# Performance work log

Measured on AMD Instinct MI355X. Metric: run time of the kernel, lower is better.

## Reference

```python
import jax, jax.numpy as jnp
import numpy as np

B, I, H = 8192, 1024, 1024

def setup_inputs() -> dict:
    key = jax.random.key(0)
    ks = jax.random.split(key, 5)
    # xavier-uniform-ish scale for weights
    sW = float(np.sqrt(6.0 / (I + H)))
    sU = float(np.sqrt(6.0 / (H + H)))
    return {
        "x": jax.random.normal(ks[0], (B, I), jnp.float32),
        "h": jax.random.normal(ks[1], (B, H), jnp.float32),
        "c": jax.random.normal(ks[2], (B, H), jnp.float32),
        # gate order along leading axis: 0=i, 1=f, 2=o, 3=c_hat
        "W": jax.random.uniform(ks[3], (4, H, I), jnp.float32, -sW, sW),
        "bW": jnp.zeros((4, H), jnp.float32),
        "U": jax.random.uniform(ks[4], (4, H, H), jnp.float32, -sU, sU),
        "bU": jnp.zeros((4, H), jnp.float32),
    }

def reference(x, h, c, W, bW, U, bU):
    # two batched GEMMs covering all 8 original Linear layers
    gx = jnp.einsum('bi,ghi->gbh', x, W) + bW[:, None, :]   # [4,B,H]
    gh = jnp.einsum('bk,ghk->gbh', h, U) + bU[:, None, :]   # [4,B,H]
    g = gx + gh
    i = jax.nn.sigmoid(g[0])
    f = jax.nn.sigmoid(g[1])
    o = jax.nn.sigmoid(g[2])
    c_hat = jnp.tanh(g[3])
    c_new = f * c + i * c_hat
    h_new = o * jnp.tanh(c_new)
    return (h_new, (h_new, c_new))
```

## Files before the change

kernel.cpp:

```cpp
#include <hip/hip_runtime.h>
#include <hip/hip_bf16.h>

typedef __hip_bfloat16 bf16;
typedef __attribute__((ext_vector_type(8))) short short8;
typedef __attribute__((ext_vector_type(4))) short short4v;
typedef __attribute__((ext_vector_type(4))) float floatx4;

#define B_DIM 8192
#define H_DIM 1024
#define KSUM 2048
#define BM 256
#define BN 256
#define BK 64
#define KT 32
#define NSLOT 10
#define SLOT_ELEMS 8192
#define CEX_STRIDE 68

union BS { bf16 b; short s; };
__device__ __forceinline__ short cvt1(float f) {
  BS u; u.b = __float2bfloat16(f); return u.s;
}
__device__ __forceinline__ short4v cvt4(float4 v) {
  short4v r;
  r[0] = cvt1(v.x); r[1] = cvt1(v.y); r[2] = cvt1(v.z); r[3] = cvt1(v.w);
  return r;
}

__device__ __forceinline__ void async_ld16(const bf16* g, bf16* lds) {
  __builtin_amdgcn_global_load_lds(
      (const __attribute__((address_space(1))) unsigned int*)g,
      (__attribute__((address_space(3))) unsigned int*)lds,
      16, 0, 0);
}

#define NX_UNITS 2097152
#define NW_UNITS 1048576
#define TOT_UNITS 6291456
__global__ __launch_bounds__(256) void cvt_pack(
    const float* __restrict__ x, const float* __restrict__ h,
    const float* __restrict__ W, const float* __restrict__ U,
    bf16* __restrict__ Ac, bf16* __restrict__ Bc) {
  const float4* const x4 = (const float4*)x;
  const float4* const h4 = (const float4*)h;
  const float4* const W4 = (const float4*)W;
  const float4* const U4 = (const float4*)U;
  short4v* const Ac4 = (short4v*)Ac;
  short4v* const Bc4 = (short4v*)Bc;

  const int stride = gridDim.x * 256;
  for (long u = blockIdx.x * 256 + threadIdx.x; u < TOT_UNITS; u += stride) {
    if (u < NX_UNITS) {
      const long r = u >> 8; const int c = (int)(u & 255);
      Ac4[r * 512 + c] = cvt4(x4[u]);
    } else if (u < 2 * NX_UNITS) {
      const long v = u - NX_UNITS;
      const long r = v >> 8; const int c = (int)(v & 255);
      Ac4[r * 512 + 256 + c] = cvt4(h4[v]);
    } else if (u < 2 * NX_UNITS + NW_UNITS) {
      const long w = u - 2 * NX_UNITS;
      const int g = (int)(w >> 18); const long hh = (w >> 8) & 1023;
      const int c = (int)(w & 255);
      Bc4[(hh * 4 + g) * 512 + c] = cvt4(W4[w]);
    } else {
      const long w = u - (2 * NX_UNITS + NW_UNITS);
      const int g = (int)(w >> 18); const long hh = (w >> 8) & 1023;
      const int c = (int)(w & 255);
      Bc4[(hh * 4 + g) * 512 + 256 + c] = cvt4(U4[w]);
    }
  }
}

__device__ __forceinline__ float sigmoidf_(float v) {
  return 1.0f / (1.0f + __expf(-v));
}
__device__ __forceinline__ float tanhf_(float v) {
  return 1.0f - 2.0f / (__expf(2.0f * v) + 1.0f);
}
__device__ __forceinline__ float getc(const float4& v, int t) {
  return t == 0 ? v.x : t == 1 ? v.y : t == 2 ? v.z : v.w;
}

__global__ __launch_bounds__(512, 2) void gemm_lstm(
    const bf16* __restrict__ Ac, const bf16* __restrict__ Bc,
    const float* __restrict__ cprev_g, const float* __restrict__ bW,
    const float* __restrict__ bU, float* __restrict__ out) {
  extern __shared__ __align__(16) char smem[];
  bf16* const ring = (bf16*)smem;
  float* const cex = (float*)smem;

  const int tid  = threadIdx.x;
  const int lane = tid & 63;
  const int wv   = tid >> 6;
  const int wm_idx = wv >> 2;
  const int wn_idx = wv & 3;

  const int blk  = blockIdx.x;
  const int xcd  = blk & 7;
  const int slot = blk >> 3;
  const int mt   = slot & 31;
  const int nt   = (xcd << 1) | (slot >> 5);
  const long m0 = (long)mt * BM;
  const long n0 = (long)nt * BN;

  const int lrow   = lane >> 3;
  const int lchunk = lane & 7;
  const int schunk = lchunk ^ lrow;
  const bf16* const aRow0 = Ac + (m0 + wv * 8 + lrow) * (long)KSUM + schunk * 8;
  const bf16* const bRow0 = Bc + (n0 + wv * 8 + lrow) * (long)KSUM + schunk * 8;

  const int col16 = lane & 15;
  const int quad  = lane >> 4;
  const int x7    = col16 & 7;
  const int bRowOff = (wn_idx & 1) << 6;

  floatx4 acc[8][4];
#pragma unroll
  for (int i = 0; i < 8; ++i)
#pragma unroll
    for (int jq = 0; jq < 4; ++jq) acc[i][jq] = (floatx4){0.f, 0.f, 0.f, 0.f};

#define STAGE_HALF(h_)                                                        \
  {                                                                           \
    const int c_ = (h_) & 3;                                                  \
    const long off_ = ((long)((c_ >> 1) * 128)) * KSUM + (long)(((h_) >> 2) * BK); \
    const bf16* s_ = ((c_ & 1) ? bRow0 : aRow0) + off_;                       \
    bf16* d_ = ring + ((h_) % NSLOT) * SLOT_ELEMS + wv * 512;                 \
    async_ld16(s_, d_);                                                       \
    async_ld16(s_ + 64L * KSUM, d_ + 4096);                                   \
  }

#define STAGE_P(p_)                                                           \
  { const int h_ = 4 * j + (p_) + 6; if (h_ < 4 * KT) STAGE_HALF(h_); }

#define RD_A(dst, rh_, s_)                                                    \
  _Pragma("unroll") for (int fi = 0; fi < 4; ++fi)                            \
    dst[fi] = *(const short8*)&rA[((rh_) * 64 + fi * 16 + col16) * 64 +       \
                                  (((((s_) << 2) + quad) ^ x7) << 3)];

#define RD_B(dst, s_)                                                         \
  _Pragma("unroll") for (int fj = 0; fj < 4; ++fj)                            \
    dst[fj] = *(const short8*)&rB[(bRowOff + fj * 16 + col16) * 64 +          \
                                  (((((s_) << 2) + quad) ^ x7) << 3)];

#define MM(accrow_, a_, b_)                                                   \
  __builtin_amdgcn_s_setprio(1);                                              \
  _Pragma("unroll") for (int fi = 0; fi < 4; ++fi)                            \
    _Pragma("unroll") for (int fj = 0; fj < 4; ++fj)                          \
      acc[(accrow_) + fi][fj] = __builtin_amdgcn_mfma_f32_16x16x32_bf16(      \
          a_[fi], b_[fj], acc[(accrow_) + fi][fj], 0, 0, 0);                  \
  __builtin_amdgcn_s_setprio(0);

#define FENCE() __builtin_amdgcn_sched_barrier(0)

#pragma unroll
  for (int h = 0; h < 6; ++h) STAGE_HALF(h);
  asm volatile("s_waitcnt vmcnt(4)" ::: "memory");
  __builtin_amdgcn_s_barrier();

#pragma unroll 1
  for (int j = 0; j < KT; ++j) {
    const bf16* const rA =
        ring + ((4 * j + 2 * wm_idx) % NSLOT) * SLOT_ELEMS;
    const bf16* const rB =
        ring + ((4 * j + 1 + ((wn_idx >> 1) << 1)) % NSLOT) * SLOT_ELEMS;
    short8 a0s0[4], a0s1[4], a1s0[4], a1s1[4], b_s0[4], b_s1[4];

    RD_A(a0s0, 0, 0) RD_B(b_s0, 0)
    FENCE();
    RD_A(a0s1, 0, 1) RD_B(b_s1, 1)
    FENCE();
    STAGE_P(0) STAGE_P(1)
    FENCE();
    MM(0, a0s0, b_s0)
    FENCE();
    RD_A(a1s0, 1, 0)
    FENCE();
    MM(0, a0s1, b_s1)
    FENCE();
    RD_A(a1s1, 1, 1)
    STAGE_P(2) STAGE_P(3)
    FENCE();
    MM(4, a1s0, b_s0)
    MM(4, a1s1, b_s1)
    if (j < KT - 2) asm volatile("s_waitcnt vmcnt(4)" ::: "memory");
    else            asm volatile("s_waitcnt vmcnt(0)" ::: "memory");
    __builtin_amdgcn_s_barrier();
  }

  const int rquad = (lane >> 4) << 2;
  const int row16 = lane & 15;
  const int tq    = lane >> 4;
  const long hglob = ((n0 + (long)(wn_idx << 6)) >> 2) + tq * 4;

  float4 bsum[4];
#pragma unroll
  for (int g = 0; g < 4; ++g) {
    const float4 a = *(const float4*)(bW + g * H_DIM + hglob);
    const float4 b = *(const float4*)(bU + g * H_DIM + hglob);
    bsum[g] = (float4){a.x + b.x, a.y + b.y, a.z + b.z, a.w + b.w};
  }

  float* wx = cex + wv * (16 * CEX_STRIDE);
  const long BH = (long)B_DIM * H_DIM;

#pragma unroll
  for (int ig = 0; ig < 8; ++ig) {
#pragma unroll
    for (int jj = 0; jj < 4; ++jj)
#pragma unroll
      for (int r = 0; r < 4; ++r)
        wx[(rquad + r) * CEX_STRIDE + jj * 16 + col16] = acc[ig][jj][r];

    float4 g4[4];
#pragma unroll
    for (int t = 0; t < 4; ++t)
      g4[t] = *(const float4*)&wx[row16 * CEX_STRIDE + (tq * 4 + t) * 4];

    const long mrow = m0 + (long)wm_idx * 128 + ig * 16 + row16;
    const float4 cp4 = *(const float4*)(cprev_g + mrow * H_DIM + hglob);

    float hn[4], cn[4];
#pragma unroll
    for (int t = 0; t < 4; ++t) {
      const float gi = g4[t].x + getc(bsum[0], t);
      const float gf = g4[t].y + getc(bsum[1], t);
      const float go = g4[t].z + getc(bsum[2], t);
      const float gg = g4[t].w + getc(bsum[3], t);
      const float I = sigmoidf_(gi);
      const float F = sigmoidf_(gf);
      const float O = sigmoidf_(go);
      const float G = tanhf_(gg);
      const float cv = F * getc(cp4, t) + I * G;
      hn[t] = O * tanhf_(cv);
      cn[t] = cv;
    }
    const float4 hn4 = {hn[0], hn[1], hn[2], hn[3]};
    const float4 cn4 = {cn[0], cn[1], cn[2], cn[3]};
    const long ob = mrow * H_DIM + hglob;
    *(float4*)(out + ob)          = hn4;
    *(float4*)(out + BH + ob)     = hn4;
    *(float4*)(out + 2 * BH + ob) = cn4;
  }
}

extern "C" void kernel_launch(void* const* d_in, const int* in_sizes, int n_in,
                              void* d_out, int out_size, void* d_ws, size_t ws_size,
                              hipStream_t stream) {
  const float* x  = (const float*)d_in[0];
  const float* h  = (const float*)d_in[1];
  const float* c  = (const float*)d_in[2];
  const float* W  = (const float*)d_in[3];
  const float* bW = (const float*)d_in[4];
  const float* U  = (const float*)d_in[5];
  const float* bU = (const float*)d_in[6];
  float* out = (float*)d_out;

  bf16* Ac = (bf16*)d_ws;
  bf16* Bc = (bf16*)((char*)d_ws + (size_t)33554432);

  static bool attr_done = false;
  if (!attr_done) {
    hipFuncSetAttribute(reinterpret_cast<const void*>(gemm_lstm),
                        hipFuncAttributeMaxDynamicSharedMemorySize, 163840);
    attr_done = true;
  }

  cvt_pack<<<4096, 256, 0, stream>>>(x, h, W, U, Ac, Bc);
  gemm_lstm<<<512, 512, 163840, stream>>>(Ac, Bc, c, bW, bU, out);
}
```

Baseline: 333.4 us.

## Shrink GEMM tile to 256x128 with BK=32 and 4-wave blocks

Changes the fused GEMM+LSTM kernel from 256x256 tiles with 8 waves and BK=64 to 256x128 tiles with 4 waves and BK=32. This doubles the grid to 1024 blocks and rebuilds the LDS ring: 9 slots of 3 buffers (A0, A1, B) with a new swizzled staging layout and fragment addressing. The goal is smaller LDS use (73.7KB) for more resident blocks and better CU balance. In exchange, B is reused across fewer rows, so global/L2 traffic per FLOP rises, and a barrier is hit every 32-wide K step. The epilogue is not shown and may not match the new wave layout.

```diff
diff --git a/kernel.cpp b/kernel.cpp
--- a/kernel.cpp
+++ b/kernel.cpp
@@ -10,11 +10,11 @@
 #define H_DIM 1024
 #define KSUM 2048
 #define BM 256
-#define BN 256
-#define BK 64
-#define KT 32
-#define NSLOT 10
-#define SLOT_ELEMS 8192
+#define BN 128
+#define BK 32
+#define KT 64
+#define NSLOT 9
+#define SLOT_ELEMS 4096
 #define CEX_STRIDE 68
 
 union BS { bf16 b; short s; };
@@ -81,7 +81,7 @@
   return t == 0 ? v.x : t == 1 ? v.y : t == 2 ? v.z : v.w;
 }
 
-__global__ __launch_bounds__(512, 2) void gemm_lstm(
+__global__ __launch_bounds__(256, 2) void gemm_lstm(
     const bf16* __restrict__ Ac, const bf16* __restrict__ Bc,
     const float* __restrict__ cprev_g, const float* __restrict__ bW,
     const float* __restrict__ bU, float* __restrict__ out) {
@@ -92,27 +92,27 @@
   const int tid  = threadIdx.x;
   const int lane = tid & 63;
   const int wv   = tid >> 6;
-  const int wm_idx = wv >> 2;
-  const int wn_idx = wv & 3;
+  const int wm_idx = wv >> 1;
+  const int wn_idx = wv & 1;
 
   const int blk  = blockIdx.x;
   const int xcd  = blk & 7;
   const int slot = blk >> 3;
   const int mt   = slot & 31;
-  const int nt   = (xcd << 1) | (slot >> 5);
+  const int nt   = (xcd << 2) | (slot >> 5);
   const long m0 = (long)mt * BM;
   const long n0 = (long)nt * BN;
 
-  const int lrow   = lane >> 3;
-  const int lchunk = lane & 7;
-  const int schunk = lchunk ^ lrow;
-  const bf16* const aRow0 = Ac + (m0 + wv * 8 + lrow) * (long)KSUM + schunk * 8;
-  const bf16* const bRow0 = Bc + (n0 + wv * 8 + lrow) * (long)KSUM + schunk * 8;
+  const int rbits = 2 * (lane >> 3) + ((lane >> 2) & 1);
+  const int csrc  = (lane & 3) ^ ((lane >> 3) & 3);
+  const bf16* const aStage = Ac + (m0 + wv * 32 + rbits) * (long)KSUM + csrc * 8;
+  const bf16* const bStage = Bc + (n0 + wv * 32 + rbits) * (long)KSUM + csrc * 8;
 
   const int col16 = lane & 15;
   const int quad  = lane >> 4;
-  const int x7    = col16 & 7;
-  const int bRowOff = (wn_idx & 1) << 6;
+  const int c16h  = col16 >> 1;
+  const int c16l  = col16 & 1;
+  const int loff  = c16h * 64 + c16l * 32 + ((quad ^ (c16h & 3)) << 3);
 
   floatx4 acc[8][4];
 #pragma unroll
@@ -120,72 +120,67 @@
 #pragma unroll
     for (int jq = 0; jq < 4; ++jq) acc[i][jq] = (floatx4){0.f, 0.f, 0.f, 0.f};
 
-#define STAGE_HALF(h_)                                                        \
+#define STAGE_SLOT(kt_, c_, sl_)                                              \
   {                                                                           \
-    const int c_ = (h_) & 3;                                                  \
-    const long off_ = ((long)((c_ >> 1) * 128)) * KSUM + (long)(((h_) >> 2) * BK); \
-    const bf16* s_ = ((c_ & 1) ? bRow0 : aRow0) + off_;                       \
-    bf16* d_ = ring + ((h_) % NSLOT) * SLOT_ELEMS + wv * 512;                 \
+    const bf16* s_ = (((c_) == 2) ? bStage                                    \
+                                  : (aStage + (long)(c_) * 128 * KSUM)) +     \
+                     (long)(kt_) * BK;                                        \
+    bf16* d_ = ring + (sl_) * SLOT_ELEMS + wv * 1024;                         \
     async_ld16(s_, d_);                                                       \
-    async_ld16(s_ + 64L * KSUM, d_ + 4096);                                   \
-  }
-
-#define STAGE_P(p_)                                                           \
-  { const int h_ = 4 * j + (p_) + 6; if (h_ < 4 * KT) STAGE_HALF(h_); }
-
-#define RD_A(dst, rh_, s_)                                                    \
+    async_ld16(s_ + 16L * KSUM, d_ + 512);                                    \
+  }
+
+#define RD_A4(lo_)                                                            \
   _Pragma("unroll") for (int fi = 0; fi < 4; ++fi)                            \
-    dst[fi] = *(const short8*)&rA[((rh_) * 64 + fi * 16 + col16) * 64 +       \
-                                  (((((s_) << 2) + quad) ^ x7) << 3)];
-
-#define RD_B(dst, s_)                                                         \
+    af[(lo_) + fi] = *(const short8*)&rA[((lo_) + fi) * 512 + loff];
+
+#define RD_B4()                                                               \
   _Pragma("unroll") for (int fj = 0; fj < 4; ++fj)                            \
-    dst[fj] = *(const short8*)&rB[(bRowOff + fj * 16 + col16) * 64 +          \
-                                  (((((s_) << 2) + quad) ^ x7) << 3)];
-
-#define MM(accrow_, a_, b_)                                                   \
+    bfr[fj] = *(const short8*)&rB[wn_idx * 2048 + fj * 512 + loff];
+
+#define MM16(lo_)                                                             \
   __builtin_amdgcn_s_setprio(1);                                              \
   _Pragma("unroll") for (int fi = 0; fi < 4; ++fi)                            \
     _Pragma("unroll") for (int fj = 0; fj < 4; ++fj)                          \
-      acc[(accrow_) + fi][fj] = __builtin_amdgcn_mfma_f32_16x16x32_bf16(      \
-          a_[fi], b_[fj], acc[(accrow_) + fi][fj], 0, 0, 0);                  \
+      acc[(lo_) + fi][fj] = __builtin_amdgcn_mfma_f32_16x16x32_bf16(          \
+          af[(lo_) + fi], bfr[fj], acc[(lo_) + fi][fj], 0, 0, 0);             \
   __builtin_amdgcn_s_setprio(0);
 
 #define FENCE() __builtin_amdgcn_sched_barrier(0)
 
 #pragma unroll
-  for (int h = 0; h < 6; ++h) STAGE_HALF(h);
-  asm volatile("s_waitcnt vmcnt(4)" ::: "memory");
+  for (int kt = 0; kt < 2; ++kt)
+#pragma unroll
+    for (int c = 0; c < 3; ++c)
+      STAGE_SLOT(kt, c, 3 * kt + c)
+  asm volatile("s_waitcnt vmcnt(6)" ::: "memory");
   __builtin_amdgcn_s_barrier();
 
+  int sb = 0;
 #pragma unroll 1
   for (int j = 0; j < KT; ++j) {
-    const bf16* const rA =
-        ring + ((4 * j + 2 * wm_idx) % NSLOT) * SLOT_ELEMS;
-    const bf16* const rB =
-        ring + ((4 * j + 1 + ((wn_idx >> 1) << 1)) % NSLOT) * SLOT_ELEMS;
-    short8 a0s0[4], a0s1[4], a1s0[4], a1s1[4], b_s0[4], b_s1[4];
-
-    RD_A(a0s0, 0, 0) RD_B(b_s0, 0)
+    const bf16* const rA = ring + (sb + wm_idx) * SLOT_ELEMS;
+    const bf16* const rB = ring + (sb + 2) * SLOT_ELEMS;
+    short8 af[8], bfr[4];
+
+    RD_B4() RD_A4(0) RD_A4(4)
     FENCE();
-    RD_A(a0s1, 0, 1) RD_B(b_s1, 1)
+    {
+      const int w = (sb >= 3) ? sb - 3 : sb + 6;
+      if (j + 2 < KT) {
+        STAGE_SLOT(j + 2, 0, w)
+        STAGE_SLOT(j + 2, 1, w + 1)
+        STAGE_SLOT(j + 2, 2, w + 2)
+      }
+    }
     FENCE();
-    STAGE_P(0) STAGE_P(1)
+    MM16(0)
     FENCE();
-    MM(0, a0s0, b_s0)
-    FENCE();
-    RD_A(a1s0, 1, 0)
-    FENCE();
-    MM(0, a0s1, b_s1)
-    FENCE();
-    RD_A(a1s1, 1, 1)
-    STAGE_P(2) STAGE_P(3)
-    FENCE();
-    MM(4, a1s0, b_s0)
-    MM(4, a1s1, b_s1)
-    if (j < KT - 2) asm volatile("s_waitcnt vmcnt(4)" ::: "memory");
+    MM16(4)
+    if (j < KT - 2) asm volatile("s_waitcnt vmcnt(6)" ::: "memory");
     else            asm volatile("s_waitcnt vmcnt(0)" ::: "memory");
     __builtin_amdgcn_s_barrier();
+    sb = (sb == 6) ? 0 : sb + 3;
   }
 
   const int rquad = (lane >> 4) << 2;
@@ -262,10 +257,10 @@
   static bool attr_done = false;
   if (!attr_done) {
     hipFuncSetAttribute(reinterpret_cast<const void*>(gemm_lstm),
-                        hipFuncAttributeMaxDynamicSharedMemorySize, 163840);
+                        hipFuncAttributeMaxDynamicSharedMemorySize, 73728);
     attr_done = true;
   }
 
   cvt_pack<<<4096, 256, 0, stream>>>(x, h, W, U, Ac, Bc);
-  gemm_lstm<<<512, 512, 163840, stream>>>(Ac, Bc, c, bW, bU, out);
-}
+  gemm_lstm<<<1024, 256, 73728, stream>>>(Ac, Bc, c, bW, bU, out);
+}
```

Measured after the change: 376.6 us. 1.13x slower.

## Load B operand directly from global into registers and shrink the LDS ring

Applied to the files above, without the earlier changes.

The B (weight) tile is no longer staged through LDS. Each wave now reads its B fragments straight from global memory into registers every K-step. Only the A tile stays in a 6-slot LDS ring, which cuts dynamic shared memory from 160 KB to 96 KB and removes the LDS writes and reads for B. In exchange, global-load latency for B sits on the critical path each iteration. The direct reads use strided 16-byte rows, and waves that share a B column both load the same data, so global traffic is duplicated.

```diff
diff --git a/kernel.cpp b/kernel.cpp
--- a/kernel.cpp
+++ b/kernel.cpp
@@ -13,7 +13,7 @@
 #define BN 256
 #define BK 64
 #define KT 32
-#define NSLOT 10
+#define NSLOT 6
 #define SLOT_ELEMS 8192
 #define CEX_STRIDE 68
 
@@ -107,12 +107,13 @@
   const int lchunk = lane & 7;
   const int schunk = lchunk ^ lrow;
   const bf16* const aRow0 = Ac + (m0 + wv * 8 + lrow) * (long)KSUM + schunk * 8;
-  const bf16* const bRow0 = Bc + (n0 + wv * 8 + lrow) * (long)KSUM + schunk * 8;
 
   const int col16 = lane & 15;
   const int quad  = lane >> 4;
   const int x7    = col16 & 7;
-  const int bRowOff = (wn_idx & 1) << 6;
+
+  const bf16* const bBase =
+      Bc + (n0 + (long)(wn_idx << 6) + col16) * (long)KSUM + quad * 8;
 
   floatx4 acc[8][4];
 #pragma unroll
@@ -120,28 +121,23 @@
 #pragma unroll
     for (int jq = 0; jq < 4; ++jq) acc[i][jq] = (floatx4){0.f, 0.f, 0.f, 0.f};
 
-#define STAGE_HALF(h_)                                                        \
+#define STAGE_A(kt_, half_, sl_)                                              \
   {                                                                           \
-    const int c_ = (h_) & 3;                                                  \
-    const long off_ = ((long)((c_ >> 1) * 128)) * KSUM + (long)(((h_) >> 2) * BK); \
-    const bf16* s_ = ((c_ & 1) ? bRow0 : aRow0) + off_;                       \
-    bf16* d_ = ring + ((h_) % NSLOT) * SLOT_ELEMS + wv * 512;                 \
+    const bf16* s_ = aRow0 + (long)(half_) * (128 * KSUM) + (long)(kt_) * BK; \
+    bf16* d_ = ring + (sl_) * SLOT_ELEMS + wv * 512;                          \
     async_ld16(s_, d_);                                                       \
     async_ld16(s_ + 64L * KSUM, d_ + 4096);                                   \
   }
-
-#define STAGE_P(p_)                                                           \
-  { const int h_ = 4 * j + (p_) + 6; if (h_ < 4 * KT) STAGE_HALF(h_); }
 
 #define RD_A(dst, rh_, s_)                                                    \
   _Pragma("unroll") for (int fi = 0; fi < 4; ++fi)                            \
     dst[fi] = *(const short8*)&rA[((rh_) * 64 + fi * 16 + col16) * 64 +       \
                                   (((((s_) << 2) + quad) ^ x7) << 3)];
 
-#define RD_B(dst, s_)                                                         \
+#define LD_B(dst, s_)                                                         \
   _Pragma("unroll") for (int fj = 0; fj < 4; ++fj)                            \
-    dst[fj] = *(const short8*)&rB[(bRowOff + fj * 16 + col16) * 64 +          \
-                                  (((((s_) << 2) + quad) ^ x7) << 3)];
+    dst[fj] = *(const short8*)(bBase + (long)fj * (16 * KSUM) + jk +          \
+                               (s_) * 32);
 
 #define MM(accrow_, a_, b_)                                                   \
   __builtin_amdgcn_s_setprio(1);                                              \
@@ -153,24 +149,31 @@
 
 #define FENCE() __builtin_amdgcn_sched_barrier(0)
 
-#pragma unroll
-  for (int h = 0; h < 6; ++h) STAGE_HALF(h);
+  STAGE_A(0, 0, 0) STAGE_A(0, 1, 1)
+  STAGE_A(1, 0, 2) STAGE_A(1, 1, 3)
   asm volatile("s_waitcnt vmcnt(4)" ::: "memory");
   __builtin_amdgcn_s_barrier();
 
+  int sa = 0;
 #pragma unroll 1
   for (int j = 0; j < KT; ++j) {
-    const bf16* const rA =
-        ring + ((4 * j + 2 * wm_idx) % NSLOT) * SLOT_ELEMS;
-    const bf16* const rB =
-        ring + ((4 * j + 1 + ((wn_idx >> 1) << 1)) % NSLOT) * SLOT_ELEMS;
+    const bf16* const rA = ring + (sa + wm_idx) * SLOT_ELEMS;
+    const long jk = (long)j * BK;
     short8 a0s0[4], a0s1[4], a1s0[4], a1s1[4], b_s0[4], b_s1[4];
 
-    RD_A(a0s0, 0, 0) RD_B(b_s0, 0)
-    FENCE();
-    RD_A(a0s1, 0, 1) RD_B(b_s1, 1)
-    FENCE();
-    STAGE_P(0) STAGE_P(1)
+    LD_B(b_s0, 0) LD_B(b_s1, 1)
+    FENCE();
+    {
+      const int w = (sa >= 2) ? sa - 2 : 4;
+      if (j + 2 < KT) {
+        STAGE_A(j + 2, 0, w)
+        STAGE_A(j + 2, 1, w + 1)
+      }
+    }
+    FENCE();
+    RD_A(a0s0, 0, 0)
+    FENCE();
+    RD_A(a0s1, 0, 1)
     FENCE();
     MM(0, a0s0, b_s0)
     FENCE();
@@ -179,13 +182,13 @@
     MM(0, a0s1, b_s1)
     FENCE();
     RD_A(a1s1, 1, 1)
-    STAGE_P(2) STAGE_P(3)
     FENCE();
     MM(4, a1s0, b_s0)
     MM(4, a1s1, b_s1)
     if (j < KT - 2) asm volatile("s_waitcnt vmcnt(4)" ::: "memory");
     else            asm volatile("s_waitcnt vmcnt(0)" ::: "memory");
     __builtin_amdgcn_s_barrier();
+    sa = (sa == 4) ? 0 : sa + 2;
   }
 
   const int rquad = (lane >> 4) << 2;
@@ -262,10 +265,10 @@
   static bool attr_done = false;
   if (!attr_done) {
     hipFuncSetAttribute(reinterpret_cast<const void*>(gemm_lstm),
-                        hipFuncAttributeMaxDynamicSharedMemorySize, 163840);
+                        hipFuncAttributeMaxDynamicSharedMemorySize, 98304);
     attr_done = true;
   }
 
   cvt_pack<<<4096, 256, 0, stream>>>(x, h, W, U, Ac, Bc);
-  gemm_lstm<<<512, 512, 163840, stream>>>(Ac, Bc, c, bW, bU, out);
-}
+  gemm_lstm<<<512, 512, 98304, stream>>>(Ac, Bc, c, bW, bU, out);
+}
```

New measurement: 420.1 us. +26.0%, slower.
